# Performance work log

Hardware: AMD Instinct MI355X
Metric: run time of the kernel (lower is better)

## Reference

```python
import jax, jax.numpy as jnp
import numpy as np

LOG_2PI = float(np.log(2.0 * np.pi))


def gaussian_log_density(samples, mean, log_squared_scale):
    inv_sigma = jnp.exp(-log_squared_scale)
    tmp = samples - mean
    return -0.5 * (tmp * tmp * inv_sigma + log_squared_scale + LOG_2PI)


def setup_inputs() -> dict:
    key = jax.random.key(0)
    k1, k2, k3, k4, k5 = jax.random.split(key, 5)
    B, L, D = 4096, 16, 512
    return {
        "data": jax.random.normal(k1, (B, D), dtype=jnp.float32),
        "reconstruction": jax.random.normal(k2, (B, D), dtype=jnp.float32),
        "z": jax.random.normal(k3, (B, L), dtype=jnp.float32),
        "z_mean": jax.random.normal(k4, (B, L), dtype=jnp.float32),
        "z_log_var": jax.random.normal(k5, (B, L), dtype=jnp.float32),
    }


def reference(data, reconstruction, z, z_mean, z_log_var):
    # reconstruction loss: mean over batch of per-sample MAE (mean over feature axis)
    recon_loss = jnp.mean(jnp.abs(data - reconstruction))

    # KL penalty: mean over batch of 0.5 * sum over latents
    summand = jnp.square(z_mean) + jnp.exp(z_log_var) - z_log_var - 1.0
    kl_loss = jnp.mean(0.5 * jnp.sum(summand, axis=1))

    # total correlation: pairwise gaussian log-density [B, B, L]
    log_qz_prob = gaussian_log_density(
        z[:, None, :], z_mean[None, :, :], z_log_var[None, :, :]
    )
    # log prod_l q(z_l): logsumexp over batch axis 1 per latent, then sum over latents
    log_qz_product = jnp.sum(jax.nn.logsumexp(log_qz_prob, axis=1), axis=1)
    # log q(z): sum over latents first, then logsumexp over batch axis
    log_qz = jax.nn.logsumexp(jnp.sum(log_qz_prob, axis=2), axis=1)
    tc_loss = jnp.mean(log_qz - log_qz_product)

    total_loss = recon_loss + kl_loss + tc_loss
    return total_loss
```

## Files before the change

kernel.cpp:

```cpp
#include <hip/hip_runtime.h>
#include <hip/hip_fp16.h>
#include <math.h>

#define BB 4096
#define LL 16
#define DD 512

#define LOG2E_F  1.4426950408889634f
#define LN2_F    0.6931471805599453f
#define LOG2PI_F 1.8378770664093453f

#define OFFC     22.942540f
#define SCALE23  8388608.0f
#define BIASF    126.94269504f

#if __has_builtin(__builtin_amdgcn_exp2f)
#define EXP2(x) __builtin_amdgcn_exp2f(x)
#else
#define EXP2(x) exp2f(x)
#endif
#if __has_builtin(__builtin_amdgcn_logf)
#define LOG2(x) __builtin_amdgcn_logf(x)
#else
#define LOG2(x) log2f(x)
#endif

typedef float f32x2 __attribute__((ext_vector_type(2)));
typedef float f32x4 __attribute__((ext_vector_type(4)));

#define COEF_F   0
#define RP_F     196608
#define KLP_F    198656
#define PART_F   268544

__device__ __forceinline__ float block_reduce(float v) {
  __shared__ float sm[4];
  __syncthreads();
#pragma unroll
  for (int off = 32; off; off >>= 1) v += __shfl_xor(v, off);
  if ((threadIdx.x & 63) == 0) sm[threadIdx.x >> 6] = v;
  __syncthreads();
  if (threadIdx.x == 0) v = (sm[0] + sm[1]) + (sm[2] + sm[3]);
  return v;
}

__global__ __launch_bounds__(256) void prep_recon_kernel(
    const float4* __restrict__ data4, const float4* __restrict__ recon4,
    const float* __restrict__ zm, const float* __restrict__ zlv,
    float* __restrict__ coef, float* __restrict__ rp,
    float* __restrict__ klp, float* __restrict__ out) {
  const int tid = threadIdx.x;
  const int b = blockIdx.x;

  if (b == 1024 && tid == 0) out[0] = 0.0f;

  {
    const int n4 = (BB * DD) / 4;
    int stride = gridDim.x * 256;
    float s = 0.0f;
    for (int k = b * 256 + tid; k < n4; k += stride) {
      float4 a = data4[k];
      float4 r = recon4[k];
      s += (fabsf(a.x - r.x) + fabsf(a.y - r.y)) +
           (fabsf(a.z - r.z) + fabsf(a.w - r.w));
    }
    float t = block_reduce(s);
    if (tid == 0) rp[b] = t * (1.0f / (float)(BB * DD));
  }

  if (b < 256) {
    const float S = 1024.0f / 65535.0f;
    int idx = b * 256 + tid;
    int j = idx >> 4;
    int l = idx & 15;
    float m = zm[idx];
    float lv = zlv[idx];
    float inv = EXP2(-lv * LOG2E_F);
    float a = -0.5f * LOG2E_F * inv;
    float c2 = -0.5f * LOG2E_F * (lv + LOG2PI_F);
    coef[j * 48 + l]      = m;
    coef[j * 48 + 16 + l] = a * S;
    coef[j * 48 + 32 + l] = (c2 + OFFC) * S;

    float kls = m * m + EXP2(lv * LOG2E_F) - lv - 1.0f;
    float s = block_reduce(kls);
    if (tid == 0) klp[b] = s * (0.5f / (float)BB);
  }
}

template <int CHUNK>
__global__ __launch_bounds__(256, 3) void tc_kernel(
    const float* __restrict__ z, const float* __restrict__ coef,
    float* __restrict__ partial) {
  __shared__ float lcoef[CHUNK * 48];
  const int tid = threadIdx.x;
  const int i0 = blockIdx.x * 1024 + tid;
  const int j0 = blockIdx.y * CHUNK;
  const float JMUL = 65535.0f * 8192.0f;
  const float JK   = -SCALE23 * (16.0f * OFFC - BIASF);

  {
    const f32x4* g4 = (const f32x4*)(coef + (size_t)j0 * 48);
    f32x4* l4 = (f32x4*)lcoef;
    for (int t = tid; t < (CHUNK * 48) / 4; t += 256) l4[t] = g4[t];
  }

  f32x2 zv[4][8];
#pragma unroll
  for (int r = 0; r < 4; ++r) {
    const f32x4* zp = (const f32x4*)(z + (size_t)(i0 + 256 * r) * 16);
#pragma unroll
    for (int q = 0; q < 4; ++q) {
      f32x4 v = zp[q];
      zv[r][2 * q]     = __builtin_shufflevector(v, v, 0, 1);
      zv[r][2 * q + 1] = __builtin_shufflevector(v, v, 2, 3);
    }
  }
#pragma unroll
  for (int r = 0; r < 4; ++r)
#pragma unroll
    for (int p = 0; p < 8; ++p) asm volatile("" : "+v"(zv[r][p]));

  union HU { unsigned u; __half2 h; };
  __half2 accH[4][8];
#pragma unroll
  for (int r = 0; r < 4; ++r)
#pragma unroll
    for (int p = 0; p < 8; ++p) { HU t; t.u = 0u; accH[r][p] = t.h; }
  float accJ[4] = {0.0f, 0.0f, 0.0f, 0.0f};

  __syncthreads();

  const float* cp = lcoef;
#pragma unroll 2
  for (int j = 0; j < CHUNK; ++j) {
    f32x2 js2[4] = {{0.0f, 0.0f}, {0.0f, 0.0f}, {0.0f, 0.0f}, {0.0f, 0.0f}};
#pragma unroll
    for (int q = 0; q < 4; ++q) {
      f32x4 m4 = *(const f32x4*)(cp + 4 * q);
      f32x4 a4 = *(const f32x4*)(cp + 16 + 4 * q);
      f32x4 c4 = *(const f32x4*)(cp + 32 + 4 * q);
      f32x2 mlo = __builtin_shufflevector(m4, m4, 0, 1);
      f32x2 mhi = __builtin_shufflevector(m4, m4, 2, 3);
      f32x2 alo = __builtin_shufflevector(a4, a4, 0, 1);
      f32x2 ahi = __builtin_shufflevector(a4, a4, 2, 3);
      f32x2 clo = __builtin_shufflevector(c4, c4, 0, 1);
      f32x2 chi = __builtin_shufflevector(c4, c4, 2, 3);
#pragma unroll
      for (int r = 0; r < 4; ++r) {
        f32x2 tlo = zv[r][2 * q] - mlo;
        f32x2 thi = zv[r][2 * q + 1] - mhi;
        f32x2 ulo = alo * tlo;
        f32x2 uhi = ahi * thi;
        f32x2 lplo = __builtin_elementwise_fma(ulo, tlo, clo);
        f32x2 lphi = __builtin_elementwise_fma(uhi, thi, chi);
        HU h0, h1;
        asm("v_cvt_pknorm_u16_f32 %0, %1, %2"
            : "=v"(h0.u) : "v"(lplo.x), "v"(lplo.y));
        asm("v_cvt_pknorm_u16_f32 %0, %1, %2"
            : "=v"(h1.u) : "v"(lphi.x), "v"(lphi.y));
        accH[r][2 * q]     = __hadd2(accH[r][2 * q], h0.h);
        accH[r][2 * q + 1] = __hadd2(accH[r][2 * q + 1], h1.h);
        js2[r] += lplo;
        js2[r] += lphi;
      }
    }
#pragma unroll
    for (int r = 0; r < 4; ++r) {
      float js = js2[r].x + js2[r].y;
      float w = fmaf(js, JMUL, JK);
      unsigned u;
      asm("v_cvt_u32_f32 %0, %1" : "=v"(u) : "v"(w));
      accJ[r] += __uint_as_float(u);
    }
    cp += 48;
  }

#pragma unroll
  for (int r = 0; r < 4; ++r) {
    const size_t b9 = ((size_t)blockIdx.y * 9) * BB + (size_t)(i0 + 256 * r);
    unsigned* up = (unsigned*)partial;
#pragma unroll
    for (int p = 0; p < 8; ++p) {
      HU t; t.h = accH[r][p];
      up[b9 + (size_t)p * BB] = t.u;
    }
    partial[b9 + (size_t)8 * BB] = accJ[r];
  }
}

__global__ __launch_bounds__(256) void reduce_kernel(
    const unsigned* __restrict__ partial, float* __restrict__ red2) {
  const int i = blockIdx.x * 256 + threadIdx.x;
  const int g = blockIdx.y;
  const unsigned* p = partial + ((size_t)g * 16 * 9) * BB + i;

  float s[17];
#pragma unroll
  for (int k = 0; k < 17; ++k) s[k] = 0.0f;

#pragma unroll 4
  for (int c = 0; c < 16; ++c) {
    const size_t cb = (size_t)c * 9 * BB;
    union HU { unsigned u; __half2 h; };
#pragma unroll
    for (int q = 0; q < 8; ++q) {
      HU t; t.u = p[cb + (size_t)q * BB];
      s[2 * q]     += __low2float(t.h);
      s[2 * q + 1] += __high2float(t.h);
    }
    s[16] += __uint_as_float(p[cb + (size_t)8 * BB]);
  }

  float* r2 = red2 + ((size_t)g * 17) * BB + i;
#pragma unroll
  for (int k = 0; k < 16; ++k)
    r2[(size_t)k * BB] = s[k] * 0.00390625f;
  r2[(size_t)16 * BB] = s[16];
}

__global__ __launch_bounds__(256) void final_kernel(
    const float* __restrict__ red2, const float* __restrict__ rp,
    const float* __restrict__ klp, float* __restrict__ out, int G) {
  const int tid = threadIdx.x;
  const int i = blockIdx.x * 256 + tid;

  float acc[17];
#pragma unroll
  for (int k = 0; k < 17; ++k) acc[k] = 0.0f;
  for (int g = 0; g < G; ++g) {
    const float* r2 = red2 + ((size_t)g * 17) * BB + i;
#pragma unroll
    for (int k = 0; k < 17; ++k) acc[k] += r2[(size_t)k * BB];
  }

  float lg = LOG2(acc[16]);
#pragma unroll
  for (int k = 0; k < 16; ++k) lg -= LOG2(acc[k]);
  float t = lg * (LN2_F / (float)BB);
  if (blockIdx.x == 0) {
#pragma unroll
    for (int q = 0; q < 8; ++q) t += rp[tid + 256 * q];
    t += klp[tid];
  }
  float s = block_reduce(t);
  if (tid == 0) atomicAdd(out, s);
}

extern "C" void kernel_launch(void* const* d_in, const int* in_sizes, int n_in,
                              void* d_out, int out_size, void* d_ws, size_t ws_size,
                              hipStream_t stream) {
  const float* data  = (const float*)d_in[0];
  const float* recon = (const float*)d_in[1];
  const float* z     = (const float*)d_in[2];
  const float* zm    = (const float*)d_in[3];
  const float* zlv   = (const float*)d_in[4];
  float* out = (float*)d_out;
  float* ws  = (float*)d_ws;

  int nc = 256;
  {
    size_t need = (size_t)PART_F + (size_t)nc * 9 * BB + (size_t)(nc / 16) * 17 * BB;
    if (need * 4 > ws_size) nc = 128;
  }
  const int G = nc / 16;

  float* coef = ws + COEF_F;
  float* rp   = ws + RP_F;
  float* klp  = ws + KLP_F;
  float* part = ws + PART_F;
  float* red2 = ws + PART_F + (size_t)nc * 9 * BB;

  hipLaunchKernelGGL(prep_recon_kernel, dim3(2048), dim3(256), 0, stream,
                     reinterpret_cast<const float4*>(data),
                     reinterpret_cast<const float4*>(recon),
                     zm, zlv, coef, rp, klp, out);
  if (nc == 256) {
    hipLaunchKernelGGL(tc_kernel<16>, dim3(4, 256), dim3(256), 0, stream,
                       z, coef, part);
  } else {
    hipLaunchKernelGGL(tc_kernel<32>, dim3(4, 128), dim3(256), 0, stream,
                       z, coef, part);
  }
  hipLaunchKernelGGL(reduce_kernel, dim3(BB / 256, G), dim3(256), 0, stream,
                     reinterpret_cast<const unsigned*>(part), red2);
  hipLaunchKernelGGL(final_kernel, dim3(BB / 256), dim3(256), 0, stream,
                     red2, rp, klp, out, G);
}
```

Baseline: 120.7 us.

## Expand quadratic coefficients, double rows per thread, and stagger per-wave LDS coefficient reads

The per-pair log-density is re-expressed as a*z^2 + b*z + c with b and c precomputed in the prep kernel. This turns the subtract, multiply and FMA sequence into two scalar FMAs per element. The TC kernel now processes 8 rows per thread instead of 4, which halves the grid in x and lowers the occupancy hint to 2. Each wave keeps its own LDS copy of the coefficients and walks j with a wave-dependent rotation, which removes the block barrier and is meant to cut LDS bank conflicts. The costs are extra register pressure and fewer resident waves, and the expanded form may lose floating-point precision when z is far from the mean.

After: 178.5 us. 47.8% more time.

```diff
diff --git a/kernel.cpp b/kernel.cpp
--- a/kernel.cpp
+++ b/kernel.cpp
@@ -25,8 +25,7 @@
 #define LOG2(x) log2f(x)
 #endif
 
-typedef float f32x2 __attribute__((ext_vector_type(2)));
-typedef float f32x4 __attribute__((ext_vector_type(4)));
+typedef float f32x4v __attribute__((ext_vector_type(4)));
 
 #define COEF_F   0
 #define RP_F     196608
@@ -78,9 +77,9 @@
     float inv = EXP2(-lv * LOG2E_F);
     float a = -0.5f * LOG2E_F * inv;
     float c2 = -0.5f * LOG2E_F * (lv + LOG2PI_F);
-    coef[j * 48 + l]      = m;
-    coef[j * 48 + 16 + l] = a * S;
-    coef[j * 48 + 32 + l] = (c2 + OFFC) * S;
+    coef[j * 48 + l]      = a * S;
+    coef[j * 48 + 16 + l] = -2.0f * a * m * S;
+    coef[j * 48 + 32 + l] = (fmaf(a, m * m, c2) + OFFC) * S;
 
     float kls = m * m + EXP2(lv * LOG2E_F) - lv - 1.0f;
     float s = block_reduce(kls);
@@ -88,96 +87,91 @@
   }
 }
 
-template <int CHUNK>
-__global__ __launch_bounds__(256, 3) void tc_kernel(
+template <int CHUNK, int R>
+__global__ __launch_bounds__(256, 2) void tc_kernel(
     const float* __restrict__ z, const float* __restrict__ coef,
     float* __restrict__ partial) {
-  __shared__ float lcoef[CHUNK * 48];
+  __shared__ float lcoef[4 * CHUNK * 48];
   const int tid = threadIdx.x;
-  const int i0 = blockIdx.x * 1024 + tid;
+  const int wave = tid >> 6;
+  const int lane = tid & 63;
+  const int i0 = blockIdx.x * (256 * R) + tid;
   const int j0 = blockIdx.y * CHUNK;
   const float JMUL = 65535.0f * 8192.0f;
   const float JK   = -SCALE23 * (16.0f * OFFC - BIASF);
 
+  float* wbase = lcoef + wave * (CHUNK * 48);
   {
-    const f32x4* g4 = (const f32x4*)(coef + (size_t)j0 * 48);
-    f32x4* l4 = (f32x4*)lcoef;
-    for (int t = tid; t < (CHUNK * 48) / 4; t += 256) l4[t] = g4[t];
-  }
-
-  f32x2 zv[4][8];
-#pragma unroll
-  for (int r = 0; r < 4; ++r) {
-    const f32x4* zp = (const f32x4*)(z + (size_t)(i0 + 256 * r) * 16);
+    const f32x4v* g4 = (const f32x4v*)(coef + (size_t)j0 * 48);
+    f32x4v* l4 = (f32x4v*)wbase;
+    for (int t = lane; t < CHUNK * 12; t += 64) l4[t] = g4[t];
+  }
+
+  float zv[R][16];
+#pragma unroll
+  for (int r = 0; r < R; ++r) {
+    const float4* zp = (const float4*)(z + (size_t)(i0 + 256 * r) * 16);
 #pragma unroll
     for (int q = 0; q < 4; ++q) {
-      f32x4 v = zp[q];
-      zv[r][2 * q]     = __builtin_shufflevector(v, v, 0, 1);
-      zv[r][2 * q + 1] = __builtin_shufflevector(v, v, 2, 3);
-    }
-  }
-#pragma unroll
-  for (int r = 0; r < 4; ++r)
-#pragma unroll
-    for (int p = 0; p < 8; ++p) asm volatile("" : "+v"(zv[r][p]));
+      float4 v = zp[q];
+      zv[r][4 * q] = v.x; zv[r][4 * q + 1] = v.y;
+      zv[r][4 * q + 2] = v.z; zv[r][4 * q + 3] = v.w;
+    }
+  }
+#pragma unroll
+  for (int r = 0; r < R; ++r)
+#pragma unroll
+    for (int p = 0; p < 16; ++p) asm volatile("" : "+v"(zv[r][p]));
 
   union HU { unsigned u; __half2 h; };
-  __half2 accH[4][8];
-#pragma unroll
-  for (int r = 0; r < 4; ++r)
+  __half2 accH[R][8];
+#pragma unroll
+  for (int r = 0; r < R; ++r)
 #pragma unroll
     for (int p = 0; p < 8; ++p) { HU t; t.u = 0u; accH[r][p] = t.h; }
-  float accJ[4] = {0.0f, 0.0f, 0.0f, 0.0f};
-
-  __syncthreads();
-
-  const float* cp = lcoef;
-#pragma unroll 2
+  float accJ[R];
+#pragma unroll
+  for (int r = 0; r < R; ++r) accJ[r] = 0.0f;
+
+  const int rot = wave * (CHUNK / 4);
   for (int j = 0; j < CHUNK; ++j) {
-    f32x2 js2[4] = {{0.0f, 0.0f}, {0.0f, 0.0f}, {0.0f, 0.0f}, {0.0f, 0.0f}};
+    const int jj = (j + rot) & (CHUNK - 1);
+    const float* cp = wbase + jj * 48;
+    float js[R];
+#pragma unroll
+    for (int r = 0; r < R; ++r) js[r] = 0.0f;
 #pragma unroll
     for (int q = 0; q < 4; ++q) {
-      f32x4 m4 = *(const f32x4*)(cp + 4 * q);
-      f32x4 a4 = *(const f32x4*)(cp + 16 + 4 * q);
-      f32x4 c4 = *(const f32x4*)(cp + 32 + 4 * q);
-      f32x2 mlo = __builtin_shufflevector(m4, m4, 0, 1);
-      f32x2 mhi = __builtin_shufflevector(m4, m4, 2, 3);
-      f32x2 alo = __builtin_shufflevector(a4, a4, 0, 1);
-      f32x2 ahi = __builtin_shufflevector(a4, a4, 2, 3);
-      f32x2 clo = __builtin_shufflevector(c4, c4, 0, 1);
-      f32x2 chi = __builtin_shufflevector(c4, c4, 2, 3);
-#pragma unroll
-      for (int r = 0; r < 4; ++r) {
-        f32x2 tlo = zv[r][2 * q] - mlo;
-        f32x2 thi = zv[r][2 * q + 1] - mhi;
-        f32x2 ulo = alo * tlo;
-        f32x2 uhi = ahi * thi;
-        f32x2 lplo = __builtin_elementwise_fma(ulo, tlo, clo);
-        f32x2 lphi = __builtin_elementwise_fma(uhi, thi, chi);
+      float4 va = *(const float4*)(cp + 4 * q);
+      float4 vb = *(const float4*)(cp + 16 + 4 * q);
+      float4 vc = *(const float4*)(cp + 32 + 4 * q);
+#pragma unroll
+      for (int r = 0; r < R; ++r) {
+        float lp0 = fmaf(fmaf(va.x, zv[r][4 * q + 0], vb.x), zv[r][4 * q + 0], vc.x);
+        float lp1 = fmaf(fmaf(va.y, zv[r][4 * q + 1], vb.y), zv[r][4 * q + 1], vc.y);
+        float lp2 = fmaf(fmaf(va.z, zv[r][4 * q + 2], vb.z), zv[r][4 * q + 2], vc.z);
+        float lp3 = fmaf(fmaf(va.w, zv[r][4 * q + 3], vb.w), zv[r][4 * q + 3], vc.w);
         HU h0, h1;
         asm("v_cvt_pknorm_u16_f32 %0, %1, %2"
-            : "=v"(h0.u) : "v"(lplo.x), "v"(lplo.y));
+            : "=v"(h0.u) : "v"(lp0), "v"(lp1));
         asm("v_cvt_pknorm_u16_f32 %0, %1, %2"
-            : "=v"(h1.u) : "v"(lphi.x), "v"(lphi.y));
+            : "=v"(h1.u) : "v"(lp2), "v"(lp3));
         accH[r][2 * q]     = __hadd2(accH[r][2 * q], h0.h);
         accH[r][2 * q + 1] = __hadd2(accH[r][2 * q + 1], h1.h);
-        js2[r] += lplo;
-        js2[r] += lphi;
+        js[r] += (lp0 + lp1) + (lp2 + lp3);
       }
     }
 #pragma unroll
-    for (int r = 0; r < 4; ++r) {
-      float js = js2[r].x + js2[r].y;
-      float w = fmaf(js, JMUL, JK);
+    for (int r = 0; r < R; ++r) {
+      float w = fmaf(js[r], JMUL, JK);
       unsigned u;
       asm("v_cvt_u32_f32 %0, %1" : "=v"(u) : "v"(w));
       accJ[r] += __uint_as_float(u);
     }
-    cp += 48;
-  }
-
-#pragma unroll
-  for (int r = 0; r < 4; ++r) {
+  }
+
+#pragma unroll
+  for (int r = 0; r < R; ++r) {
     const size_t b9 = ((size_t)blockIdx.y * 9) * BB + (size_t)(i0 + 256 * r);
     unsigned* up = (unsigned*)partial;
 #pragma unroll
@@ -276,10 +270,10 @@
                      reinterpret_cast<const float4*>(recon),
                      zm, zlv, coef, rp, klp, out);
   if (nc == 256) {
-    hipLaunchKernelGGL(tc_kernel<16>, dim3(4, 256), dim3(256), 0, stream,
+    hipLaunchKernelGGL((tc_kernel<16, 8>), dim3(2, 256), dim3(256), 0, stream,
                        z, coef, part);
   } else {
-    hipLaunchKernelGGL(tc_kernel<32>, dim3(4, 128), dim3(256), 0, stream,
+    hipLaunchKernelGGL((tc_kernel<32, 8>), dim3(2, 128), dim3(256), 0, stream,
                        z, coef, part);
   }
   hipLaunchKernelGGL(reduce_kernel, dim3(BB / 256, G), dim3(256), 0, stream,
```
